# Optimization experiments

Hardware: AMD Instinct MI355X
Metric: run time of the kernel (lower is better)

Reference implementation:

```python
import jax, jax.numpy as jnp
import numpy as np

B, C, W, H = 2, 64, 96, 96
C8 = C // 8


def setup_inputs() -> dict:
    key = jax.random.key(0)
    ks = jax.random.split(key, 8)
    return {
        "x": jax.random.normal(ks[0], (B, C, W, H), dtype=jnp.float32),
        "Wq": jax.random.normal(ks[1], (C8, C), dtype=jnp.float32) * 0.05,
        "bq": jax.random.normal(ks[2], (C8,), dtype=jnp.float32) * 0.05,
        "Wk": jax.random.normal(ks[3], (C8, C), dtype=jnp.float32) * 0.05,
        "bk": jax.random.normal(ks[4], (C8,), dtype=jnp.float32) * 0.05,
        "Wv": jax.random.normal(ks[5], (C, C), dtype=jnp.float32) * 0.05,
        "bv": jax.random.normal(ks[6], (C,), dtype=jnp.float32) * 0.05,
        "gamma": jax.random.normal(ks[7], (1,), dtype=jnp.float32),
    }


def reference(x, Wq, bq, Wk, bk, Wv, bv, gamma):
    b, c, w, h = x.shape
    n = w * h
    xf = x.reshape(b, c, n)  # [B, C, N]
    # 1x1 convs are channel-mixing matmuls over flattened spatial dim
    q = jnp.einsum('oc,bcn->bno', Wq, xf) + bq          # [B, N, C//8] (proj_query, permuted)
    k = jnp.einsum('oc,bcn->bon', Wk, xf) + bk[:, None]  # [B, C//8, N] (proj_key)
    energy = jnp.einsum('bno,bom->bnm', q, k)            # [B, N, N]
    # torch softmax over dim=1 (the query index), NOT the usual dim=-1
    attn = jax.nn.softmax(energy, axis=1)                # [B, N, N]
    v = jnp.einsum('oc,bcn->bon', Wv, xf) + bv[:, None]  # [B, C, N]
    # bmm(V, attn.permute(0,2,1)): out[b,c,m] = sum_n V[b,c,n] * attn[b,m,n]
    out = jnp.einsum('bcn,bmn->bcm', v, attn).reshape(b, c, w, h)
    return gamma * out + x
```

## Files before the change

### kernel.cpp

```cpp
#include <hip/hip_runtime.h>
#include <math.h>

#define NN 9216
#define LOG2E 1.4426950408889634f

typedef __attribute__((ext_vector_type(8))) __bf16 bf16x8;
typedef __attribute__((ext_vector_type(16))) float f32x16;
typedef __attribute__((ext_vector_type(4))) unsigned int u32x4;

#define MFMA32(a,b,c) __builtin_amdgcn_mfma_f32_32x32x16_bf16(a,b,c,0,0,0)

#if __has_builtin(__builtin_amdgcn_exp2f)
#define EXP2(x) __builtin_amdgcn_exp2f(x)
#else
#define EXP2(x) exp2f(x)
#endif

__device__ __forceinline__ bf16x8 zero8() {
    bf16x8 z;
    #pragma unroll
    for (int i = 0; i < 8; i++) z[i] = (__bf16)0.0f;
    return z;
}

__device__ __forceinline__ unsigned int pk2(float a, float b) {
    unsigned short ua = __builtin_bit_cast(unsigned short, (__bf16)a);
    unsigned short ub = __builtin_bit_cast(unsigned short, (__bf16)b);
    return (unsigned int)ua | ((unsigned int)ub << 16);
}

__device__ __forceinline__ void plane_swap(unsigned int &a, unsigned int &b) {
    asm("v_permlane32_swap_b32 %0, %1" : "+v"(a), "+v"(b));
}

__device__ __forceinline__ void cp16(void* lds, const void* g) {
    __builtin_amdgcn_global_load_lds(
        (const __attribute__((address_space(1))) unsigned int*)g,
        (__attribute__((address_space(3))) unsigned int*)lds, 16, 0, 0);
}

#define OFF_QB 0
#define OFF_KB 294912
#define OFF_VB 589824
#define OFF_DP 2949120
#define OFF_PARTS 3096576
#define WS_NEED 21970944ULL

__global__ __launch_bounds__(256) void qkv_kernel(
    const float* __restrict__ x,
    const float* __restrict__ Wq, const float* __restrict__ bq,
    const float* __restrict__ Wk, const float* __restrict__ bk,
    const float* __restrict__ Wv, const float* __restrict__ bv,
    __bf16* __restrict__ QB, __bf16* __restrict__ KB, __bf16* __restrict__ VB)
{
    __shared__ float wvs[1024], wqs[512], wks[512], bvs[16], bqs[8], bks[8];
    int tid = threadIdx.x;
    int z = blockIdx.z, b = blockIdx.y;
    for (int i = tid; i < 1024; i += 256) wvs[i] = Wv[z*1024 + i];
    if (z == 0)
        for (int i = tid; i < 512; i += 256) { wqs[i] = Wq[i]; wks[i] = Wk[i]; }
    if (tid < 16) bvs[tid] = bv[z*16 + tid];
    if (tid < 8)  { bqs[tid] = bq[tid]; bks[tid] = bk[tid]; }
    __syncthreads();

    int n = blockIdx.x * 256 + tid;

    float xc[64];
    #pragma unroll
    for (int c = 0; c < 64; c++) xc[c] = x[((size_t)(b*64 + c))*NN + n];

    float v[16];
    #pragma unroll
    for (int o = 0; o < 16; o++) v[o] = bvs[o];
    #pragma unroll
    for (int c = 0; c < 64; c++) {
        float xv = xc[c];
        #pragma unroll
        for (int o = 0; o < 16; o++) v[o] = fmaf(wvs[o*64+c], xv, v[o]);
    }
    #pragma unroll
    for (int o = 0; o < 16; o++)
        VB[((size_t)(b*64 + z*16 + o))*NN + n] = (__bf16)v[o];

    if (z == 0) {
        float q[8], k[8];
        #pragma unroll
        for (int o = 0; o < 8; o++) { q[o] = bqs[o]; k[o] = bks[o]; }
        #pragma unroll
        for (int c = 0; c < 64; c++) {
            float xv = xc[c];
            #pragma unroll
            for (int o = 0; o < 8; o++) {
                q[o] = fmaf(wqs[o*64+c], xv, q[o]);
                k[o] = fmaf(wks[o*64+c], xv, k[o]);
            }
        }
        bf16x8 qv, kv;
        #pragma unroll
        for (int o = 0; o < 8; o++) {
            qv[o] = (__bf16)(q[o] * LOG2E);
            kv[o] = (__bf16)k[o];
        }
        *(bf16x8*)(QB + ((size_t)b*NN + n)*8) = qv;
        *(bf16x8*)(KB + ((size_t)b*NN + n)*8) = kv;
    }
}

__global__ __launch_bounds__(256) void stats_kernel(
    const __bf16* __restrict__ QB, const __bf16* __restrict__ KB,
    float* __restrict__ Dp)
{
    __shared__ float Dl[4][32];
    int tid = threadIdx.x;
    int lane = tid & 63, w = tid >> 6;
    int l31 = lane & 31, h = lane >> 5;
    int b = blockIdx.y, z = blockIdx.z;
    int n0 = blockIdx.x * 32;

    f32x16 Z16;
    #pragma unroll
    for (int r = 0; r < 16; r++) Z16[r] = 0.0f;

    bf16x8 kf = zero8();
    if (lane < 32)
        kf = *(const bf16x8*)(KB + ((size_t)b*NN + n0 + l31)*8);

    float Dacc[16];
    #pragma unroll
    for (int r = 0; r < 16; r++) Dacc[r] = 0.0f;

    const __bf16* Qb = QB + (size_t)b*NN*8;
    int mbase = z*4608 + w*1152;
    for (int it = 0; it < 36; it++) {
        bf16x8 qf = zero8();
        if (lane < 32)
            qf = *(const bf16x8*)(Qb + (size_t)(mbase + it*32 + l31)*8);
        f32x16 e = MFMA32(kf, qf, Z16);
        #pragma unroll
        for (int r = 0; r < 16; r++) Dacc[r] += EXP2(e[r]);
    }
    #pragma unroll
    for (int r = 0; r < 16; r++) {
        #pragma unroll
        for (int mask = 1; mask < 32; mask <<= 1)
            Dacc[r] += __shfl_xor(Dacc[r], mask);
    }
    if (l31 == 0) {
        #pragma unroll
        for (int r = 0; r < 16; r++)
            Dl[w][(r&3) + 8*(r>>2) + 4*h] = Dacc[r];
    }
    __syncthreads();
    if (tid < 32)
        Dp[((size_t)z*2 + b)*NN + n0 + tid] =
            Dl[0][tid] + Dl[1][tid] + Dl[2][tid] + Dl[3][tid];
}

__global__ __launch_bounds__(256) void fold_kernel(
    const float* __restrict__ Dp, const float* __restrict__ gamma_p,
    __bf16* __restrict__ VB)
{
    __shared__ float Rl[32];
    int tid = threadIdx.x;
    int b = blockIdx.y;
    int n0 = blockIdx.x * 32;
    if (tid < 32)
        Rl[tid] = gamma_p[0] / (Dp[(size_t)b*NN + n0 + tid] +
                                Dp[((size_t)2 + b)*NN + n0 + tid]);
    __syncthreads();

    int c = tid >> 2, j = tid & 3;
    __bf16* ptr = VB + ((size_t)(b*64 + c))*NN + n0 + j*8;
    bf16x8 vv = *(bf16x8*)ptr;
    #pragma unroll
    for (int i = 0; i < 8; i++)
        vv[i] = (__bf16)((float)vv[i] * Rl[j*8 + i]);
    *(bf16x8*)ptr = vv;
}

__global__ __launch_bounds__(256) void init_kernel(
    const float* __restrict__ x, float* __restrict__ out)
{
    int i = blockIdx.x*256 + threadIdx.x;
    ((float4*)out)[i] = ((const float4*)x)[i];
}

__global__ __launch_bounds__(256) void pv_kernel(
    const __bf16* __restrict__ QB, const __bf16* __restrict__ KB,
    const __bf16* __restrict__ VB, float* __restrict__ out,
    __bf16* __restrict__ parts)
{
    __shared__ __bf16 klin[2][64*8];
    __shared__ __bf16 vbuf[2][64*64];

    int tid = threadIdx.x;
    int lane = tid & 63, w = tid >> 6;
    int l31 = lane & 31, h = lane >> 5;
    int b = blockIdx.y, s = blockIdx.z;
    int mw = blockIdx.x * 128 + w * 32;

    f32x16 Z16;
    #pragma unroll
    for (int r = 0; r < 16; r++) Z16[r] = 0.0f;

    bf16x8 qf = zero8();
    if (lane < 32)
        qf = *(const bf16x8*)(QB + ((size_t)b*NN + mw + l31)*8);

    f32x16 acc[2];
    acc[0] = Z16; acc[1] = Z16;

#define STAGE(bi, stq) do {                                                   \
    int n0_ = s*1152 + (stq)*64;                                              \
    _Pragma("unroll")                                                         \
    for (int i_ = 0; i_ < 2; i_++) {                                          \
        int p2_ = tid + i_*256;                                               \
        int c_ = p2_ >> 3, h7_ = p2_ & 7;                                     \
        int xc_ = h7_ ^ (c_ & 7);                                             \
        cp16((char*)vbuf[bi] + i_*4096 + w*1024,                              \
             VB + ((size_t)(b*64 + c_))*NN + n0_ + xc_*8);                    \
    }                                                                         \
    if (w == 0)                                                               \
        cp16((char*)klin[bi], KB + ((size_t)b*NN + n0_ + lane)*8);            \
} while (0)

    STAGE(0, 0);

    for (int st = 0; st < 18; st++) {
        int bi = st & 1;
        __syncthreads();
        if (st < 17) {
            if (bi == 0) STAGE(1, st+1); else STAGE(0, st+1);
        }
        const __bf16* kl = klin[bi];
        char* vb = (char*)vbuf[bi];

        #pragma unroll
        for (int nt = 0; nt < 2; nt++) {
            bf16x8 kfr = zero8();
            if (lane < 32)
                kfr = *(const bf16x8*)(kl + (nt*32 + l31)*8);

            f32x16 e = MFMA32(kfr, qf, Z16);
            float pf[16];
            #pragma unroll
            for (int r = 0; r < 16; r++) pf[r] = EXP2(e[r]);
            unsigned int u[8];
            #pragma unroll
            for (int q = 0; q < 8; q++) u[q] = pk2(pf[2*q], pf[2*q+1]);
            plane_swap(u[0], u[2]); plane_swap(u[1], u[3]);
            plane_swap(u[4], u[6]); plane_swap(u[5], u[7]);
            u32x4 t0 = {u[0], u[1], u[2], u[3]};
            u32x4 t1 = {u[4], u[5], u[6], u[7]};
            bf16x8 pa[2];
            pa[0] = __builtin_bit_cast(bf16x8, t0);
            pa[1] = __builtin_bit_cast(bf16x8, t1);

            #pragma unroll
            for (int ks = 0; ks < 2; ks++) {
                #pragma unroll
                for (int ct = 0; ct < 2; ct++) {
                    int c = ct*32 + l31;
                    bf16x8 bfr = *(const bf16x8*)(vb + c*128 +
                        ((nt*64 + ks*32 + h*16) ^ ((c & 7) << 4)));
                    acc[ct] = MFMA32(pa[ks], bfr, acc[ct]);
                }
            }
        }
    }

    if (parts != nullptr) {
        __bf16* pp = parts + ((size_t)(s*2 + b))*64*NN;
        #pragma unroll
        for (int ct = 0; ct < 2; ct++) {
            int c = ct*32 + l31;
            __bf16* row = pp + (size_t)c*NN + mw + 4*h;
            #pragma unroll
            for (int q = 0; q < 4; q++) {
                uint2 v2;
                v2.x = pk2(acc[ct][4*q],   acc[ct][4*q+1]);
                v2.y = pk2(acc[ct][4*q+2], acc[ct][4*q+3]);
                *(uint2*)(row + q*8) = v2;
            }
        }
    } else {
        #pragma unroll
        for (int ct = 0; ct < 2; ct++) {
            int c = ct*32 + l31;
            #pragma unroll
            for (int r = 0; r < 16; r++) {
                int m = mw + (r&3) + 8*(r>>2) + 4*h;
                atomicAdd(out + ((size_t)(b*64 + c))*NN + m, (float)acc[ct][r]);
            }
        }
    }
}

__global__ __launch_bounds__(256) void reduce_kernel(
    const float* __restrict__ x, const __bf16* __restrict__ parts,
    float* __restrict__ out)
{
    size_t f0 = ((size_t)blockIdx.x*256 + threadIdx.x) * 8;
    float o[8];
    float4 a = *(const float4*)(x + f0);
    float4 c = *(const float4*)(x + f0 + 4);
    o[0]=a.x; o[1]=a.y; o[2]=a.z; o[3]=a.w;
    o[4]=c.x; o[5]=c.y; o[6]=c.z; o[7]=c.w;
    #pragma unroll
    for (int sIdx = 0; sIdx < 8; sIdx++) {
        bf16x8 p = *(const bf16x8*)(parts + (size_t)sIdx*(128*NN) + f0);
        #pragma unroll
        for (int j = 0; j < 8; j++) o[j] += (float)p[j];
    }
    float4 r0 = make_float4(o[0],o[1],o[2],o[3]);
    float4 r1 = make_float4(o[4],o[5],o[6],o[7]);
    *(float4*)(out + f0) = r0;
    *(float4*)(out + f0 + 4) = r1;
}

extern "C" void kernel_launch(void* const* d_in, const int* in_sizes, int n_in,
                              void* d_out, int out_size, void* d_ws, size_t ws_size,
                              hipStream_t stream) {
    const float* x     = (const float*)d_in[0];
    const float* Wq    = (const float*)d_in[1];
    const float* bq    = (const float*)d_in[2];
    const float* Wk    = (const float*)d_in[3];
    const float* bk    = (const float*)d_in[4];
    const float* Wv    = (const float*)d_in[5];
    const float* bv    = (const float*)d_in[6];
    const float* gamma = (const float*)d_in[7];
    float* out = (float*)d_out;
    char* ws   = (char*)d_ws;

    __bf16* QB = (__bf16*)(ws + OFF_QB);
    __bf16* KB = (__bf16*)(ws + OFF_KB);
    __bf16* VB = (__bf16*)(ws + OFF_VB);
    float*  Dp = (float*)(ws + OFF_DP);

    qkv_kernel<<<dim3(36, 2, 4), 256, 0, stream>>>(x, Wq, bq, Wk, bk, Wv, bv, QB, KB, VB);
    stats_kernel<<<dim3(288, 2, 2), 256, 0, stream>>>(QB, KB, Dp);
    fold_kernel<<<dim3(288, 2), 256, 0, stream>>>(Dp, gamma, VB);

    if (ws_size >= WS_NEED) {
        __bf16* parts = (__bf16*)(ws + OFF_PARTS);
        pv_kernel<<<dim3(72, 2, 8), 256, 0, stream>>>(QB, KB, VB, out, parts);
        reduce_kernel<<<dim3(576), 256, 0, stream>>>(x, parts, out);
    } else {
        init_kernel<<<dim3(1152), 256, 0, stream>>>(x, out);
        pv_kernel<<<dim3(72, 2, 8), 256, 0, stream>>>(QB, KB, VB, out, nullptr);
    }
}
```

Measured before the change: 106.3 us.

## Split stats over four query chunks, halve pv block size, batch QK MFMAs

The stats kernel now splits the query range into four chunks instead of two, writing four partial denominators that fold_kernel sums. pv_kernel moves to 128-thread blocks covering 64 queries, doubling the grid so more blocks can run at once. Inside each stage, pv_kernel issues both QK^T MFMAs up front, computes both exp tiles, then runs the PV MFMAs under raised wave priority. The partials buffer now aliases the Dp region, which is safe only because fold finishes reading Dp before pv writes partials. The cost is more redundant K/V staging per query and extra partial-denominator traffic.

Measured after the change: 111.3 us. +4.7%, slower.

```diff
diff --git a/kernel.cpp b/kernel.cpp
--- a/kernel.cpp
+++ b/kernel.cpp
@@ -43,8 +43,8 @@
 #define OFF_KB 294912
 #define OFF_VB 589824
 #define OFF_DP 2949120
-#define OFF_PARTS 3096576
-#define WS_NEED 21970944ULL
+#define OFF_PARTS 2949120
+#define WS_NEED 21823488ULL
 
 __global__ __launch_bounds__(256) void qkv_kernel(
     const float* __restrict__ x,
@@ -130,8 +130,8 @@
     for (int r = 0; r < 16; r++) Dacc[r] = 0.0f;
 
     const __bf16* Qb = QB + (size_t)b*NN*8;
-    int mbase = z*4608 + w*1152;
-    for (int it = 0; it < 36; it++) {
+    int mbase = z*2304 + w*576;
+    for (int it = 0; it < 18; it++) {
         bf16x8 qf = zero8();
         if (lane < 32)
             qf = *(const bf16x8*)(Qb + (size_t)(mbase + it*32 + l31)*8);
@@ -152,7 +152,7 @@
     }
     __syncthreads();
     if (tid < 32)
-        Dp[((size_t)z*2 + b)*NN + n0 + tid] =
+        Dp[((size_t)(z*2 + b))*NN + n0 + tid] =
             Dl[0][tid] + Dl[1][tid] + Dl[2][tid] + Dl[3][tid];
 }
 
@@ -164,9 +164,13 @@
     int tid = threadIdx.x;
     int b = blockIdx.y;
     int n0 = blockIdx.x * 32;
-    if (tid < 32)
-        Rl[tid] = gamma_p[0] / (Dp[(size_t)b*NN + n0 + tid] +
-                                Dp[((size_t)2 + b)*NN + n0 + tid]);
+    if (tid < 32) {
+        float d = 0.0f;
+        #pragma unroll
+        for (int zz = 0; zz < 4; zz++)
+            d += Dp[((size_t)(zz*2 + b))*NN + n0 + tid];
+        Rl[tid] = gamma_p[0] / d;
+    }
     __syncthreads();
 
     int c = tid >> 2, j = tid & 3;
@@ -185,7 +189,7 @@
     ((float4*)out)[i] = ((const float4*)x)[i];
 }
 
-__global__ __launch_bounds__(256) void pv_kernel(
+__global__ __launch_bounds__(128) void pv_kernel(
     const __bf16* __restrict__ QB, const __bf16* __restrict__ KB,
     const __bf16* __restrict__ VB, float* __restrict__ out,
     __bf16* __restrict__ parts)
@@ -197,7 +201,7 @@
     int lane = tid & 63, w = tid >> 6;
     int l31 = lane & 31, h = lane >> 5;
     int b = blockIdx.y, s = blockIdx.z;
-    int mw = blockIdx.x * 128 + w * 32;
+    int mw = blockIdx.x * 64 + w * 32;
 
     f32x16 Z16;
     #pragma unroll
@@ -213,11 +217,11 @@
 #define STAGE(bi, stq) do {                                                   \
     int n0_ = s*1152 + (stq)*64;                                              \
     _Pragma("unroll")                                                         \
-    for (int i_ = 0; i_ < 2; i_++) {                                          \
-        int p2_ = tid + i_*256;                                               \
+    for (int i_ = 0; i_ < 4; i_++) {                                          \
+        int p2_ = tid + i_*128;                                               \
         int c_ = p2_ >> 3, h7_ = p2_ & 7;                                     \
         int xc_ = h7_ ^ (c_ & 7);                                             \
-        cp16((char*)vbuf[bi] + i_*4096 + w*1024,                              \
+        cp16((char*)vbuf[bi] + i_*2048 + w*1024,                              \
              VB + ((size_t)(b*64 + c_))*NN + n0_ + xc_*8);                    \
     }                                                                         \
     if (w == 0)                                                               \
@@ -235,13 +239,18 @@
         const __bf16* kl = klin[bi];
         char* vb = (char*)vbuf[bi];
 
+        bf16x8 kfr0 = zero8(), kfr1 = zero8();
+        if (lane < 32) {
+            kfr0 = *(const bf16x8*)(kl + l31*8);
+            kfr1 = *(const bf16x8*)(kl + (32 + l31)*8);
+        }
+        f32x16 e0 = MFMA32(kfr0, qf, Z16);
+        f32x16 e1 = MFMA32(kfr1, qf, Z16);
+
+        bf16x8 pa[2][2];
         #pragma unroll
         for (int nt = 0; nt < 2; nt++) {
-            bf16x8 kfr = zero8();
-            if (lane < 32)
-                kfr = *(const bf16x8*)(kl + (nt*32 + l31)*8);
-
-            f32x16 e = MFMA32(kfr, qf, Z16);
+            const f32x16& e = nt ? e1 : e0;
             float pf[16];
             #pragma unroll
             for (int r = 0; r < 16; r++) pf[r] = EXP2(e[r]);
@@ -252,21 +261,23 @@
             plane_swap(u[4], u[6]); plane_swap(u[5], u[7]);
             u32x4 t0 = {u[0], u[1], u[2], u[3]};
             u32x4 t1 = {u[4], u[5], u[6], u[7]};
-            bf16x8 pa[2];
-            pa[0] = __builtin_bit_cast(bf16x8, t0);
-            pa[1] = __builtin_bit_cast(bf16x8, t1);
-
-            #pragma unroll
-            for (int ks = 0; ks < 2; ks++) {
+            pa[nt][0] = __builtin_bit_cast(bf16x8, t0);
+            pa[nt][1] = __builtin_bit_cast(bf16x8, t1);
+        }
+
+        __builtin_amdgcn_s_setprio(1);
+        #pragma unroll
+        for (int nt = 0; nt < 2; nt++)
+            #pragma unroll
+            for (int ks = 0; ks < 2; ks++)
                 #pragma unroll
                 for (int ct = 0; ct < 2; ct++) {
                     int c = ct*32 + l31;
                     bf16x8 bfr = *(const bf16x8*)(vb + c*128 +
                         ((nt*64 + ks*32 + h*16) ^ ((c & 7) << 4)));
-                    acc[ct] = MFMA32(pa[ks], bfr, acc[ct]);
+                    acc[ct] = MFMA32(pa[nt][ks], bfr, acc[ct]);
                 }
-            }
-        }
+        __builtin_amdgcn_s_setprio(0);
     }
 
     if (parts != nullptr) {
@@ -338,15 +349,15 @@
     float*  Dp = (float*)(ws + OFF_DP);
 
     qkv_kernel<<<dim3(36, 2, 4), 256, 0, stream>>>(x, Wq, bq, Wk, bk, Wv, bv, QB, KB, VB);
-    stats_kernel<<<dim3(288, 2, 2), 256, 0, stream>>>(QB, KB, Dp);
+    stats_kernel<<<dim3(288, 2, 4), 256, 0, stream>>>(QB, KB, Dp);
     fold_kernel<<<dim3(288, 2), 256, 0, stream>>>(Dp, gamma, VB);
 
     if (ws_size >= WS_NEED) {
         __bf16* parts = (__bf16*)(ws + OFF_PARTS);
-        pv_kernel<<<dim3(72, 2, 8), 256, 0, stream>>>(QB, KB, VB, out, parts);
+        pv_kernel<<<dim3(144, 2, 8), 128, 0, stream>>>(QB, KB, VB, out, parts);
         reduce_kernel<<<dim3(576), 256, 0, stream>>>(x, parts, out);
     } else {
         init_kernel<<<dim3(1152), 256, 0, stream>>>(x, out);
-        pv_kernel<<<dim3(72, 2, 8), 256, 0, stream>>>(QB, KB, VB, out, nullptr);
-    }
-}
+        pv_kernel<<<dim3(144, 2, 8), 128, 0, stream>>>(QB, KB, VB, out, nullptr);
+    }
+}
```
